# Kernel optimization log

Hardware: AMD Instinct MI355X
Metric: run time of the kernel (lower is better)

## Reference

```python
import jax, jax.numpy as jnp
import numpy as np

XLIM = 10.0
N_BINS = 200
LATTICE = 12.42
N_O, N_H = 64, 128
T, R = 1000, 8


def setup_inputs() -> dict:
    key = jax.random.key(0)
    k1, k2 = jax.random.split(key)
    n = N_O + N_H
    stacked_radii = jax.random.uniform(k1, (T, R, n, 3), dtype=jnp.float32) * LATTICE
    lattices = jnp.full((3,), LATTICE, dtype=jnp.float32)
    gt_rdf = jax.random.uniform(k2, (3, N_BINS), dtype=jnp.float32)
    idx_O = jnp.arange(N_O, dtype=jnp.int32)
    idx_H = jnp.arange(N_H, dtype=jnp.int32) + N_O
    return {"stacked_radii": stacked_radii, "lattices": lattices,
            "gt_rdf": gt_rdf, "idx_O": idx_O, "idx_H": idx_H}


def reference(stacked_radii, lattices, gt_rdf, idx_O, idx_H):
    bins = jnp.linspace(1e-6, XLIM, N_BINS + 1, dtype=jnp.float32)
    # np.histogram normalization: rho * (4/3)pi (r_hi^3 - r_lo^3)
    shell = (4.0 / 3.0) * np.pi * (bins[1:] ** 3 - bins[:-1] ** 3)
    vol = jnp.prod(lattices)
    # wrap positions into the box (data_seq / L % 1 * L)
    x = stacked_radii / lattices % 1.0 * lattices
    x = jnp.transpose(x, (1, 0, 2, 3))  # [R, T, N, 3]

    def pair_rdf(x_rep, i0, i1):
        x0 = x_rep[:, i0]  # [T, n0, 3]
        x1 = x_rep[:, i1]  # [T, n1, 3]
        # all-pairs minimum-image distance under PBC
        delta = jnp.abs(x0[:, :, None, :] - x1[:, None, :, :])  # [T, n0, n1, 3]
        delta = jnp.where(delta > 0.5 * lattices, delta - lattices, delta)
        d = jnp.sqrt(jnp.sum(delta ** 2, axis=-1)).ravel()
        n_pairs = d.shape[0]  # includes zeros, matches original rho
        mask = (d != 0.0) & (d >= bins[0]) & (d <= bins[-1])
        bidx = jnp.clip(jnp.searchsorted(bins, d, side='right') - 1, 0, N_BINS - 1)
        hist = jax.ops.segment_sum(mask.astype(jnp.float32), bidx, num_segments=N_BINS)
        rho = n_pairs / vol
        return hist / (rho * shell)  # [N_BINS]

    pairs = [(idx_O, idx_O), (idx_H, idx_H), (idx_H, idx_O)]  # OO, HH, HO
    # sequential over replicas (like the original python loop) to bound memory
    rdfs = [jax.lax.map(lambda xr, i0=i0, i1=i1: pair_rdf(xr, i0, i1), x)
            for (i0, i1) in pairs]  # each [R, N_BINS]
    maes = jnp.stack([XLIM * jnp.mean(jnp.abs(r - g), axis=-1)
                      for r, g in zip(rdfs, gt_rdf)], axis=0)  # [3, R]
    max_maes = jnp.max(maes, axis=0)  # [R]
    rdf_stack = jnp.concatenate(rdfs, axis=-1)  # [R, 3*N_BINS]
    return rdf_stack, max_maes
```

## Files before the change

### kernel.cpp

```cpp
#include <hip/hip_runtime.h>
#include <math.h>

#define NUM_T   1000
#define NUM_R   8
#define NBINS   200
#define FPB     2
#define NCOPY   8
#define HSTR    601
#define TTSZ    224

__device__ __forceinline__ float approx_sqrt(float x) {
    float r; asm("v_sqrt_f32 %0, %1" : "=v"(r) : "v"(x)); return r;
}
__device__ __forceinline__ float fract_(float x) {
#if __has_builtin(__builtin_amdgcn_fractf)
    return __builtin_amdgcn_fractf(x);
#else
    return x - floorf(x);
#endif
}

__global__ __launch_bounds__(256) void rdf_hist_kernel(
    const float* __restrict__ radii,
    const float* __restrict__ lat,
    unsigned int* __restrict__ gh)
{
    #pragma clang fp contract(off)
    __shared__ float4 posOx[96], posH0[96], posH1[96];
    __shared__ float TT[TTSZ];
    __shared__ unsigned int hist[NCOPY * HSTR];

    const int tid = threadIdx.x;

    if (tid < TTSZ) {
        float v;
        if (tid <= 200) {
            float b;
            if (tid < NBINS) {
                const double step = (10.0 - 1e-6) / 200.0;
                b = (float)(1e-6 + (double)tid * step);
            } else {
                b = __uint_as_float(__float_as_uint(10.0f) + 1u);
            }
            unsigned lo = 0u, hi = 0x7F800000u;
            while (lo < hi) {
                unsigned mid = (lo + hi) >> 1;
                if (sqrtf(__uint_as_float(mid)) >= b) hi = mid; else lo = mid + 1;
            }
            v = __uint_as_float(lo);
        } else {
            v = __uint_as_float(0x7F800000u);
        }
        TT[tid] = v;
    }
    for (int i = tid; i < NCOPY * HSTR; i += 256) hist[i] = 0u;

    const float Lx = lat[0], Ly = lat[1], Lz = lat[2];
    __syncthreads();

    const unsigned T0b = __float_as_uint(TT[0]);
    const unsigned Rng = __float_as_uint(TT[200]) - T0b;
    const int      hc  = ((tid >> 3) & (NCOPY - 1)) * HSTR;

#define PAIR(PI, PJ, TOFF, W)                                                \
    {                                                                        \
        float tx = (PI).x - (PJ).x;                                          \
        float ty = (PI).y - (PJ).y;                                          \
        float tz = (PI).z - (PJ).z;                                          \
        float ax = fminf(fabsf(tx), Lx - fabsf(tx));                         \
        float ay = fminf(fabsf(ty), Ly - fabsf(ty));                         \
        float az = fminf(fabsf(tz), Lz - fabsf(tz));                         \
        float s  = (ax*ax + ay*ay) + az*az;                                  \
        float z  = approx_sqrt(s * 400.0f);                                  \
        int   k  = (int)z;                                                   \
        float m  = fract_(z);                                                \
        bool amb = fabsf(m - 0.5f) > 0.49980f;                               \
        if (__builtin_expect(__any(amb), 0)) {                               \
            float tlo = TT[k], thi = TT[k + 1];                              \
            k += ((s >= thi) ? 1 : 0) - ((s < tlo) ? 1 : 0);                 \
        }                                                                    \
        bool inr = (__float_as_uint(s) - T0b) < Rng;                         \
        int  kk  = inr ? ((TOFF) + k) : 600;                                 \
        atomicAdd(&hist[hc + kk], (W));                                      \
    }

    const int rep   = blockIdx.x & (NUM_R - 1);
    const int chunk = blockIdx.x / NUM_R;
    const int l     = tid & 63;
    const int q     = tid >> 6;

    float rvx = 0.f, rvy = 0.f, rvz = 0.f;
    {
        const float* s0 = radii + ((size_t)(chunk * FPB) * NUM_R + rep) * (192 * 3);
        if (tid < 192) { rvx = s0[tid*3+0]; rvy = s0[tid*3+1]; rvz = s0[tid*3+2]; }
    }

    #pragma unroll 1
    for (int f = 0; f < FPB; ++f) {
        __syncthreads();
        if (tid < 192) {
            float ux = rvx / Lx; ux -= floorf(ux);
            float uy = rvy / Ly; uy -= floorf(uy);
            float uz = rvz / Lz; uz -= floorf(uz);
            float4 p = make_float4(ux*Lx, uy*Ly, uz*Lz, 0.0f);
            if (tid < 64)       { posOx[tid] = p;  if (tid < 32) posOx[tid+64] = p; }
            else if (tid < 128) { int h = tid-64;  posH0[h] = p; if (h < 32) posH0[h+64] = p; }
            else                { int h = tid-128; posH1[h] = p; if (h < 32) posH1[h+64] = p; }
        }
        __syncthreads();

        if (f + 1 < FPB && tid < 192) {
            const float* s1 = radii + ((size_t)(chunk * FPB + f + 1) * NUM_R + rep) * (192 * 3);
            rvx = s1[tid*3+0]; rvy = s1[tid*3+1]; rvz = s1[tid*3+2];
        }

        const float4 piO = posOx[l];
        const float4 pi0 = posH0[l];
        const float4 pi1 = posH1[l];
        const int jb = l + q + 1;

        #pragma unroll
        for (int it = 0; it < 7; ++it) { float4 pj = posOx[jb + 4*it]; PAIR(piO, pj, 0, 2u); }
        if (q < 3 || l < 32)           { float4 pj = posOx[jb + 28];   PAIR(piO, pj, 0, 2u); }

        #pragma unroll
        for (int it = 0; it < 7; ++it) { float4 pj = posH0[jb + 4*it]; PAIR(pi0, pj, 200, 2u); }
        if (q < 3 || l < 32)           { float4 pj = posH0[jb + 28];   PAIR(pi0, pj, 200, 2u); }

        #pragma unroll
        for (int it = 0; it < 7; ++it) { float4 pj = posH1[jb + 4*it]; PAIR(pi1, pj, 200, 2u); }
        if (q < 3 || l < 32)           { float4 pj = posH1[jb + 28];   PAIR(pi1, pj, 200, 2u); }

        #pragma unroll 4
        for (int jj = 0; jj < 16; ++jj) {
            float4 pj = posH1[q * 16 + jj];
            PAIR(pi0, pj, 200, 2u);
        }
        #pragma unroll 4
        for (int jj = 0; jj < 16; ++jj) {
            float4 pj = posOx[q * 16 + jj];
            PAIR(pi0, pj, 400, 1u);
            PAIR(pi1, pj, 400, 1u);
        }
    }
#undef PAIR

    __syncthreads();
    for (int i = tid; i < 3 * NBINS; i += 256) {
        unsigned int v = 0;
        #pragma unroll
        for (int c = 0; c < NCOPY; ++c) v += hist[c * HSTR + i];
        if (v) atomicAdd(&gh[rep * 3 * NBINS + i], v);
    }
}

__global__ __launch_bounds__(256) void rdf_final_kernel(
    const unsigned int* __restrict__ gh,
    const float* __restrict__ gt,
    const float* __restrict__ lat,
    float* __restrict__ out)
{
    #pragma clang fp contract(off)
    const int rep = blockIdx.x;
    const int tid = threadIdx.x;
    __shared__ float bins[NBINS + 1];
    __shared__ float red[256];

    for (int i = tid; i <= NBINS; i += 256) {
        const double step = (10.0 - 1e-6) / 200.0;
        bins[i] = (i == NBINS) ? 10.0f : (float)(1e-6 + (double)i * step);
    }
    __syncthreads();

    const float vol = (lat[0] * lat[1]) * lat[2];
    const float C   = 4.18879020478639053f;
    const int npairs[3] = { NUM_T*64*64, NUM_T*128*128, NUM_T*128*64 };

    float maxmae = -3.0e38f;
    for (int p = 0; p < 3; ++p) {
        float diff = 0.0f;
        if (tid < NBINS) {
            float b0 = bins[tid], b1 = bins[tid + 1];
            float shell = C * (b1*b1*b1 - b0*b0*b0);
            float rho = (float)npairs[p] / vol;
            float g = (float)gh[(rep*3 + p)*NBINS + tid] / (rho * shell);
            out[rep*3*NBINS + p*NBINS + tid] = g;
            diff = fabsf(g - gt[p*NBINS + tid]);
        }
        red[tid] = diff;
        __syncthreads();
        for (int s = 128; s > 0; s >>= 1) {
            if (tid < s) red[tid] += red[tid + s];
            __syncthreads();
        }
        if (tid == 0) {
            float mae = 10.0f * (red[0] / 200.0f);
            if (mae > maxmae) maxmae = mae;
        }
        __syncthreads();
    }
    if (tid == 0) out[NUM_R*3*NBINS + rep] = maxmae;
}

extern "C" void kernel_launch(void* const* d_in, const int* in_sizes, int n_in,
                              void* d_out, int out_size, void* d_ws, size_t ws_size,
                              hipStream_t stream) {
    const float* radii = (const float*)d_in[0];
    const float* lat   = (const float*)d_in[1];
    const float* gt    = (const float*)d_in[2];
    unsigned int* gh   = (unsigned int*)d_ws;

    hipMemsetAsync(gh, 0, NUM_R * 3 * NBINS * sizeof(unsigned int), stream);

    dim3 grid(NUM_R * (NUM_T / FPB));
    hipLaunchKernelGGL(rdf_hist_kernel, grid, dim3(256), 0, stream,
                       radii, lat, gh);
    hipLaunchKernelGGL(rdf_final_kernel, dim3(NUM_R), dim3(256), 0, stream,
                       gh, gt, lat, (float*)d_out);
}
```

Baseline: 106.7 us.

## Interleave 16 packed 16-bit histogram copies by lane column to cut LDS conflicts

Replaces the 8 strided per-group histogram copies with 16 lane-interleaved copies (indexed by tid&15) and packs two 16-bit bin counts into each 32-bit LDS word. Out-of-range and zero distances now land in padded dummy bins instead of going through a range check, which removes that compare and select from the inner loop. The goal is to spread atomic traffic across LDS banks and cut contention on the hot histogram. In exchange, the final reduction reads 16 words per bin with shifts, and correctness relies on per-column counts staying below 65536.

```diff
diff --git a/kernel.cpp b/kernel.cpp
--- a/kernel.cpp
+++ b/kernel.cpp
@@ -5,9 +5,9 @@
 #define NUM_R   8
 #define NBINS   200
 #define FPB     2
-#define NCOPY   8
-#define HSTR    601
 #define TTSZ    224
+#define TYSTR   218
+#define HWORDS  5232
 
 __device__ __forceinline__ float approx_sqrt(float x) {
     float r; asm("v_sqrt_f32 %0, %1" : "=v"(r) : "v"(x)); return r;
@@ -28,7 +28,7 @@
     #pragma clang fp contract(off)
     __shared__ float4 posOx[96], posH0[96], posH1[96];
     __shared__ float TT[TTSZ];
-    __shared__ unsigned int hist[NCOPY * HSTR];
+    __shared__ unsigned int hist[HWORDS];
 
     const int tid = threadIdx.x;
 
@@ -53,16 +53,14 @@
         }
         TT[tid] = v;
     }
-    for (int i = tid; i < NCOPY * HSTR; i += 256) hist[i] = 0u;
+    for (int i = tid; i < HWORDS; i += 256) hist[i] = 0u;
 
     const float Lx = lat[0], Ly = lat[1], Lz = lat[2];
     __syncthreads();
 
-    const unsigned T0b = __float_as_uint(TT[0]);
-    const unsigned Rng = __float_as_uint(TT[200]) - T0b;
-    const int      hc  = ((tid >> 3) & (NCOPY - 1)) * HSTR;
-
-#define PAIR(PI, PJ, TOFF, W)                                                \
+    const int col = tid & 15;
+
+#define PAIR(PI, PJ, TBASE, W)                                               \
     {                                                                        \
         float tx = (PI).x - (PJ).x;                                          \
         float ty = (PI).y - (PJ).y;                                          \
@@ -78,16 +76,20 @@
         if (__builtin_expect(__any(amb), 0)) {                               \
             float tlo = TT[k], thi = TT[k + 1];                              \
             k += ((s >= thi) ? 1 : 0) - ((s < tlo) ? 1 : 0);                 \
+            if (k < 0) k = 216;                                              \
         }                                                                    \
-        bool inr = (__float_as_uint(s) - T0b) < Rng;                         \
-        int  kk  = inr ? ((TOFF) + k) : 600;                                 \
-        atomicAdd(&hist[hc + kk], (W));                                      \
+        int w = (TBASE) + ((k >> 1) << 4);                                   \
+        unsigned val = (unsigned)(W) << ((k & 1) << 4);                      \
+        atomicAdd(&hist[w], val);                                            \
     }
 
     const int rep   = blockIdx.x & (NUM_R - 1);
     const int chunk = blockIdx.x / NUM_R;
     const int l     = tid & 63;
     const int q     = tid >> 6;
+    const int tbOO  = col;
+    const int tbHH  = col + (109 << 4);
+    const int tbHO  = col + (218 << 4);
 
     float rvx = 0.f, rvy = 0.f, rvz = 0.f;
     {
@@ -120,37 +122,46 @@
         const int jb = l + q + 1;
 
         #pragma unroll
-        for (int it = 0; it < 7; ++it) { float4 pj = posOx[jb + 4*it]; PAIR(piO, pj, 0, 2u); }
-        if (q < 3 || l < 32)           { float4 pj = posOx[jb + 28];   PAIR(piO, pj, 0, 2u); }
-
-        #pragma unroll
-        for (int it = 0; it < 7; ++it) { float4 pj = posH0[jb + 4*it]; PAIR(pi0, pj, 200, 2u); }
-        if (q < 3 || l < 32)           { float4 pj = posH0[jb + 28];   PAIR(pi0, pj, 200, 2u); }
-
-        #pragma unroll
-        for (int it = 0; it < 7; ++it) { float4 pj = posH1[jb + 4*it]; PAIR(pi1, pj, 200, 2u); }
-        if (q < 3 || l < 32)           { float4 pj = posH1[jb + 28];   PAIR(pi1, pj, 200, 2u); }
+        for (int it = 0; it < 7; ++it) { float4 pj = posOx[jb + 4*it]; PAIR(piO, pj, tbOO, 2u); }
+        if (q < 3 || l < 32)           { float4 pj = posOx[jb + 28];   PAIR(piO, pj, tbOO, 2u); }
+
+        #pragma unroll
+        for (int it = 0; it < 7; ++it) { float4 pj = posH0[jb + 4*it]; PAIR(pi0, pj, tbHH, 2u); }
+        if (q < 3 || l < 32)           { float4 pj = posH0[jb + 28];   PAIR(pi0, pj, tbHH, 2u); }
+
+        #pragma unroll
+        for (int it = 0; it < 7; ++it) { float4 pj = posH1[jb + 4*it]; PAIR(pi1, pj, tbHH, 2u); }
+        if (q < 3 || l < 32)           { float4 pj = posH1[jb + 28];   PAIR(pi1, pj, tbHH, 2u); }
 
         #pragma unroll 4
         for (int jj = 0; jj < 16; ++jj) {
             float4 pj = posH1[q * 16 + jj];
-            PAIR(pi0, pj, 200, 2u);
+            PAIR(pi0, pj, tbHH, 2u);
         }
         #pragma unroll 4
         for (int jj = 0; jj < 16; ++jj) {
             float4 pj = posOx[q * 16 + jj];
-            PAIR(pi0, pj, 400, 1u);
-            PAIR(pi1, pj, 400, 1u);
+            PAIR(pi0, pj, tbHO, 1u);
+            PAIR(pi1, pj, tbHO, 1u);
         }
     }
 #undef PAIR
 
     __syncthreads();
-    for (int i = tid; i < 3 * NBINS; i += 256) {
-        unsigned int v = 0;
-        #pragma unroll
-        for (int c = 0; c < NCOPY; ++c) v += hist[c * HSTR + i];
-        if (v) atomicAdd(&gh[rep * 3 * NBINS + i], v);
+    for (int idx = tid; idx < 3 * NBINS; idx += 256) {
+        const int p    = idx / 200;
+        const int b    = idx - p * 200;
+        const int pr   = p * TYSTR + b;
+        const int base = (pr >> 1) << 4;
+        const int sh   = (b & 1) << 4;
+        const int c0   = idx & 15;
+        unsigned sum = 0;
+        #pragma unroll
+        for (int c = 0; c < 16; ++c) {
+            unsigned wrd = hist[base + ((c0 + c) & 15)];
+            sum += (wrd >> sh) & 0xFFFFu;
+        }
+        if (sum) atomicAdd(&gh[rep * 3 * NBINS + idx], sum);
     }
 }
 
```

Measured after the change: 107.6 us. About the same (+0.8%).
